# Kernel optimization log

Hardware: AMD Instinct MI355X
Metric: run time of the kernel (lower is better)

Reference implementation:

```python
import jax, jax.numpy as jnp
import numpy as np
import math

CN = [64, 128, 256, 512]
KV = 960  # sum(CN)
B, H, W = 8, 64, 64
HW = H * W
EPS_IN = 1e-5   # InstanceNorm2d eps
EPS_NORM = 1e-12  # F.normalize eps


def _conv(x, w, groups, pad):
    # x: NCHW, w: OIHW (I = C_in/groups)
    return jax.lax.conv_general_dilated(
        x, w, window_strides=(1, 1), padding=pad,
        feature_group_count=groups,
        dimension_numbers=('NCHW', 'OIHW', 'NCHW'))


def _l2norm(x):
    n = jnp.sqrt(jnp.sum(x * x, axis=-1, keepdims=True))
    return x / jnp.maximum(n, EPS_NORM)


def _inorm(a):
    # InstanceNorm2d(affine=False): normalize over last two dims per (b, head)
    mu = jnp.mean(a, axis=(-2, -1), keepdims=True)
    var = jnp.mean((a - mu) ** 2, axis=(-2, -1), keepdims=True)
    return (a - mu) * jax.lax.rsqrt(var + EPS_IN)


def setup_inputs() -> dict:
    key = jax.random.key(0)
    ks = iter(jax.random.split(key, 32))
    d = {}
    d['emb1'] = jax.random.normal(next(ks), (B, CN[0], H, W), jnp.float32)
    d['emb2'] = jax.random.normal(next(ks), (B, CN[1], H, W), jnp.float32)
    d['emb3'] = jax.random.normal(next(ks), (B, CN[2], H, W), jnp.float32)
    d['emb4'] = jax.random.normal(next(ks), (B, CN[3], H, W), jnp.float32)
    d['emb_all'] = jax.random.normal(next(ks), (B, KV, H, W), jnp.float32)
    s = 0.05
    for i, c in enumerate(CN, 1):
        d[f'wm{i}'] = jax.random.normal(next(ks), (c, c, 1, 1), jnp.float32) * s
        d[f'wq{i}'] = jax.random.normal(next(ks), (c, 2, 3, 3), jnp.float32) * s  # groups=c//2
        d[f'wp{i}'] = jax.random.normal(next(ks), (c, c, 1, 1), jnp.float32) * s
    d['wmk'] = jax.random.normal(next(ks), (KV, KV, 1, 1), jnp.float32) * s
    d['wmv'] = jax.random.normal(next(ks), (KV, KV, 1, 1), jnp.float32) * s
    d['wk'] = jax.random.normal(next(ks), (KV, 1, 3, 3), jnp.float32) * s  # depthwise
    d['wv'] = jax.random.normal(next(ks), (KV, 1, 3, 3), jnp.float32) * s
    return d


def reference(emb1, emb2, emb3, emb4, emb_all,
              wm1, wq1, wp1, wm2, wq2, wp2, wm3, wq3, wp3, wm4, wq4, wp4,
              wmk, wmv, wk, wv):
    b, _, h, w = emb1.shape
    scale = 1.0 / math.sqrt(KV)

    def make_q(emb, wm, wq, c):
        q = _conv(_conv(emb, wm, 1, 'VALID'), wq, c // 2, 'SAME')
        q = q.reshape(b, 1, c, h * w)  # head=1
        return _l2norm(q)

    k = _conv(_conv(emb_all, wmk, 1, 'VALID'), wk, KV, 'SAME').reshape(b, 1, KV, h * w)
    v = _conv(_conv(emb_all, wmv, 1, 'VALID'), wv, KV, 'SAME').reshape(b, 1, KV, h * w)
    k = _l2norm(k)

    outs = []
    for emb, wm, wq, wp, c in ((emb1, wm1, wq1, wp1, CN[0]),
                               (emb2, wm2, wq2, wp2, CN[1]),
                               (emb3, wm3, wq3, wp3, CN[2]),
                               (emb4, wm4, wq4, wp4, CN[3])):
        q = make_q(emb, wm, wq, c)                         # b 1 c hw
        attn = jnp.einsum('bhcn,bhdn->bhcd', q, k) * scale  # b 1 c KV
        probs = jax.nn.softmax(_inorm(attn), axis=-1)
        out = jnp.einsum('bhcd,bhdn->bhcn', probs, v)       # b 1 c hw
        out = out.mean(axis=1).reshape(b, c, h, w)          # head mean (head=1)
        outs.append(_conv(out, wp, 1, 'VALID'))
    return tuple(outs)
```

## Files before the change

### kernel.cpp

```cpp
#include <hip/hip_runtime.h>
#include <hip/hip_bf16.h>
#include <math.h>

typedef long long i64;
typedef __hip_bfloat16 bf16;

#define HW 4096
#define KVC 960
#define BATCH 8

using bf8 = __attribute__((ext_vector_type(8))) short;
using f32x4 = __attribute__((ext_vector_type(4))) float;

__device__ __forceinline__ float bf2f(unsigned short u) {
    union { unsigned int i; float f; } c; c.i = ((unsigned int)u) << 16; return c.f;
}
__device__ __forceinline__ float tof(bf16 v) { return __bfloat162float(v); }
__device__ __forceinline__ unsigned short f2bs(float f) {
    bf16 h = __float2bfloat16(f); return *reinterpret_cast<unsigned short*>(&h);
}
__device__ __forceinline__ unsigned short tobs(float f) { return f2bs(f); }
__device__ __forceinline__ unsigned short tobs(bf16 v) { return *reinterpret_cast<unsigned short*>(&v); }
__device__ __forceinline__ void store1(float* p, float v) { *p = v; }
__device__ __forceinline__ void store1(bf16* p, float v) { *p = __float2bfloat16(v); }

__device__ __forceinline__ void gl_lds16(const void* g, void* l) {
    __builtin_amdgcn_global_load_lds(
        (const __attribute__((address_space(1))) void*)g,
        (__attribute__((address_space(3))) void*)l,
        16, 0, 0);
}

template<typename TC>
__global__ __launch_bounds__(256)
void gemm_bt(const bf16* __restrict__ A, int lda, i64 aBatch,
             const bf16* __restrict__ B, int ldb, i64 bBatch,
             TC* __restrict__ C, int ldc, i64 cBatch,
             int M, int N, int K, float alpha)
{
    __shared__ __align__(16) short As[128 * 32];
    __shared__ __align__(16) short Bs[128 * 32];

    const int bz = blockIdx.z;
    const int m0 = blockIdx.y * 128;
    const int n0 = blockIdx.x * 128;
    const int tid  = threadIdx.x;
    const int lane = tid & 63;
    const int wave = tid >> 6;
    const int wm = (wave & 1) * 64;
    const int wn = (wave >> 1) * 64;
    const int quad = lane >> 4;
    const int l16  = lane & 15;

    const bf16* Ab = A + (i64)bz * aBatch;
    const bf16* Bb = B + (i64)bz * bBatch;

    const int srow = lane >> 2;
    const int scol = (lane & 3) * 8;

    int ar0 = m0 + wave * 16 + srow;       if (ar0 >= M) ar0 = M - 1;
    int ar1 = m0 + 64 + wave * 16 + srow;  if (ar1 >= M) ar1 = M - 1;
    int br0 = n0 + wave * 16 + srow;       if (br0 >= N) br0 = N - 1;
    int br1 = n0 + 64 + wave * 16 + srow;  if (br1 >= N) br1 = N - 1;
    const bf16* pa0 = Ab + (i64)ar0 * lda + scol;
    const bf16* pa1 = Ab + (i64)ar1 * lda + scol;
    const bf16* pb0 = Bb + (i64)br0 * ldb + scol;
    const bf16* pb1 = Bb + (i64)br1 * ldb + scol;

    short* la0 = As + wave * 512;
    short* la1 = As + 2048 + wave * 512;
    short* lb0 = Bs + wave * 512;
    short* lb1 = Bs + 2048 + wave * 512;

    f32x4 acc[4][4] = {};

    for (int k0 = 0; k0 < K; k0 += 32) {
        gl_lds16(pa0 + k0, la0);
        gl_lds16(pa1 + k0, la1);
        gl_lds16(pb0 + k0, lb0);
        gl_lds16(pb1 + k0, lb1);
        __syncthreads();

        bf8 af[4], bfr[4];
        #pragma unroll
        for (int mt = 0; mt < 4; ++mt)
            af[mt] = *(const bf8*)(As + (wm + mt * 16 + l16) * 32 + quad * 8);
        #pragma unroll
        for (int nt = 0; nt < 4; ++nt)
            bfr[nt] = *(const bf8*)(Bs + (wn + nt * 16 + l16) * 32 + quad * 8);
        #pragma unroll
        for (int mt = 0; mt < 4; ++mt)
            #pragma unroll
            for (int nt = 0; nt < 4; ++nt)
                acc[mt][nt] = __builtin_amdgcn_mfma_f32_16x16x32_bf16(
                    af[mt], bfr[nt], acc[mt][nt], 0, 0, 0);
        __syncthreads();
    }

    const i64 cb = (i64)bz * cBatch;
    #pragma unroll
    for (int mt = 0; mt < 4; ++mt) {
        #pragma unroll
        for (int r = 0; r < 4; ++r) {
            const int row = m0 + wm + mt * 16 + quad * 4 + r;
            if (row >= M) continue;
            const i64 rb = cb + (i64)row * ldc;
            #pragma unroll
            for (int nt = 0; nt < 4; ++nt) {
                const int col = n0 + wn + nt * 16 + l16;
                if (col < N) store1(C + rb + col, alpha * acc[mt][nt][r]);
            }
        }
    }
}

template<typename T>
__global__ __launch_bounds__(256)
void transpose_to_bt(const T* __restrict__ in, bf16* __restrict__ outT, int C)
{
    __shared__ unsigned short t[64][66];
    const int b  = blockIdx.z;
    const int n0 = blockIdx.x * 64;
    const int c0 = blockIdx.y * 64;
    const int tx = threadIdx.x & 63, ty = threadIdx.x >> 6;
    const T* ip = in + ((i64)b * C + c0) * (i64)HW + n0;
    #pragma unroll
    for (int i = 0; i < 16; ++i) {
        const int r = ty + i * 4;
        t[r][tx] = tobs(ip[(i64)r * HW + tx]);
    }
    __syncthreads();
    bf16* op = outT + ((i64)b * HW + n0) * (i64)C + c0;
    #pragma unroll
    for (int i = 0; i < 16; ++i) {
        const int r = ty + i * 4;
        *(unsigned short*)(op + (i64)r * C + tx) = t[tx][r];
    }
}

__global__ __launch_bounds__(256)
void cvt_weights(const float* __restrict__ s0, const float* __restrict__ s1,
                 const float* __restrict__ s2, const float* __restrict__ s3,
                 const float* __restrict__ s4, const float* __restrict__ s5,
                 const float* __restrict__ s6, const float* __restrict__ s7,
                 const float* __restrict__ s8, const float* __restrict__ s9,
                 bf16* __restrict__ wb)
{
    const int i = (blockIdx.x * 256 + threadIdx.x) * 4;
    if (i >= 2539520) return;
    const float* src; int off;
    if      (i <  921600) { src = s0; off = 0;       }
    else if (i < 1843200) { src = s1; off = 921600;  }
    else if (i < 1847296) { src = s2; off = 1843200; }
    else if (i < 1863680) { src = s3; off = 1847296; }
    else if (i < 1929216) { src = s4; off = 1863680; }
    else if (i < 2191360) { src = s5; off = 1929216; }
    else if (i < 2195456) { src = s6; off = 2191360; }
    else if (i < 2211840) { src = s7; off = 2195456; }
    else if (i < 2277376) { src = s8; off = 2211840; }
    else                  { src = s9; off = 2277376; }
    const float4 v = *(const float4*)(src + (i - off));
    ushort4 o;
    o.x = f2bs(v.x); o.y = f2bs(v.y); o.z = f2bs(v.z); o.w = f2bs(v.w);
    *(ushort4*)((unsigned short*)wb + i) = o;
}

template<bool NORM>
__global__ __launch_bounds__(256)
void dw3x3_fused(const bf16* __restrict__ in, const float* __restrict__ w,
                 bf16* __restrict__ out, int C)
{
    __shared__ __align__(16) unsigned short img[4096];
    __shared__ float red[4];
    __shared__ float sinv;
    const int bc = blockIdx.x;
    const int c = bc % C;
    const int tid = threadIdx.x;
    const int lane = tid & 63, wave = tid >> 6;
    const bf16* ip = in + (i64)bc * HW;
    gl_lds16(ip + wave * 512 + lane * 8, img + wave * 512);
    gl_lds16(ip + (4 + wave) * 512 + lane * 8, img + (4 + wave) * 512);

    const float* wp9 = w + c * 9;
    float wr[9];
    #pragma unroll
    for (int i = 0; i < 9; ++i) wr[i] = wp9[i];
    __syncthreads();

    const int x0 = (tid & 15) * 4, y0 = (tid >> 4) * 4;
    float fin[6][6];
    #pragma unroll
    for (int r = 0; r < 6; ++r) {
        const int yy = y0 - 1 + r;
        const int yc = (yy < 0) ? 0 : (yy > 63 ? 63 : yy);
        const bool yok = (yy >= 0) && (yy <= 63);
        #pragma unroll
        for (int cc = 0; cc < 6; ++cc) {
            const int xx = x0 - 1 + cc;
            const int xc = (xx < 0) ? 0 : (xx > 63 ? 63 : xx);
            const float v = bf2f(img[yc * 64 + xc]);
            fin[r][cc] = (yok && xx >= 0 && xx <= 63) ? v : 0.f;
        }
    }

    float o[4][4];
    float ss = 0.f;
    #pragma unroll
    for (int r = 0; r < 4; ++r) {
        #pragma unroll
        for (int cc = 0; cc < 4; ++cc) {
            float s = 0.f;
            #pragma unroll
            for (int dy = 0; dy < 3; ++dy)
                #pragma unroll
                for (int dx = 0; dx < 3; ++dx)
                    s = fmaf(wr[dy * 3 + dx], fin[r + dy][cc + dx], s);
            o[r][cc] = s;
            ss = fmaf(s, s, ss);
        }
    }

    float inv = 1.f;
    if (NORM) {
        #pragma unroll
        for (int off = 32; off > 0; off >>= 1) ss += __shfl_down(ss, off);
        const int wid = tid >> 6;
        if (lane == 0) red[wid] = ss;
        __syncthreads();
        if (tid == 0) {
            const float t = red[0] + red[1] + red[2] + red[3];
            sinv = 1.0f / fmaxf(sqrtf(t), 1e-12f);
        }
        __syncthreads();
        inv = sinv;
    }

    bf16* op = out + (i64)bc * HW;
    #pragma unroll
    for (int r = 0; r < 4; ++r) {
        ushort4 pk;
        pk.x = f2bs(o[r][0] * inv);
        pk.y = f2bs(o[r][1] * inv);
        pk.z = f2bs(o[r][2] * inv);
        pk.w = f2bs(o[r][3] * inv);
        *(ushort4*)(op + (y0 + r) * 64 + x0) = pk;
    }
}

__global__ __launch_bounds__(256)
void gconv3x3_fused(const bf16* __restrict__ in, const float* __restrict__ w,
                    bf16* __restrict__ outAll, int C, int cstart)
{
    __shared__ __align__(16) unsigned short img[8192];
    __shared__ float red[2][4];
    __shared__ float sinv[2];
    const int nb = C >> 1;
    const int b = blockIdx.x / nb;
    const int g = blockIdx.x % nb;
    const int tid = threadIdx.x, lane = tid & 63, wave = tid >> 6;
    const bf16* ip = in + ((i64)b * C + 2 * g) * HW;
    #pragma unroll
    for (int it = 0; it < 4; ++it)
        gl_lds16(ip + (it * 4 + wave) * 512 + lane * 8, img + (it * 4 + wave) * 512);

    const float* wp = w + g * 36;
    float wr[36];
    #pragma unroll
    for (int i = 0; i < 36; ++i) wr[i] = wp[i];
    __syncthreads();

    const int x0 = (tid & 15) * 4, y0 = (tid >> 4) * 4;
    float fin[2][6][6];
    #pragma unroll
    for (int ic = 0; ic < 2; ++ic) {
        #pragma unroll
        for (int r = 0; r < 6; ++r) {
            const int yy = y0 - 1 + r;
            const int yc = (yy < 0) ? 0 : (yy > 63 ? 63 : yy);
            const bool yok = (yy >= 0) && (yy <= 63);
            #pragma unroll
            for (int cc = 0; cc < 6; ++cc) {
                const int xx = x0 - 1 + cc;
                const int xc = (xx < 0) ? 0 : (xx > 63 ? 63 : xx);
                const float v = bf2f(img[ic * 4096 + yc * 64 + xc]);
                fin[ic][r][cc] = (yok && xx >= 0 && xx <= 63) ? v : 0.f;
            }
        }
    }

    float o[2][4][4];
    float ss0 = 0.f, ss1 = 0.f;
    #pragma unroll
    for (int oc = 0; oc < 2; ++oc) {
        #pragma unroll
        for (int r = 0; r < 4; ++r) {
            #pragma unroll
            for (int cc = 0; cc < 4; ++cc) {
                float s = 0.f;
                #pragma unroll
                for (int ic = 0; ic < 2; ++ic)
                    #pragma unroll
                    for (int dy = 0; dy < 3; ++dy)
                        #pragma unroll
                        for (int dx = 0; dx < 3; ++dx)
                            s = fmaf(wr[oc * 18 + ic * 9 + dy * 3 + dx],
                                     fin[ic][r + dy][cc + dx], s);
                o[oc][r][cc] = s;
                if (oc == 0) ss0 = fmaf(s, s, ss0); else ss1 = fmaf(s, s, ss1);
            }
        }
    }

    #pragma unroll
    for (int off = 32; off > 0; off >>= 1) {
        ss0 += __shfl_down(ss0, off);
        ss1 += __shfl_down(ss1, off);
    }
    const int wid = tid >> 6;
    if (lane == 0) { red[0][wid] = ss0; red[1][wid] = ss1; }
    __syncthreads();
    if (tid == 0) {
        const float t0 = red[0][0] + red[0][1] + red[0][2] + red[0][3];
        const float t1 = red[1][0] + red[1][1] + red[1][2] + red[1][3];
        sinv[0] = 1.0f / fmaxf(sqrtf(t0), 1e-12f);
        sinv[1] = 1.0f / fmaxf(sqrtf(t1), 1e-12f);
    }
    __syncthreads();

    #pragma unroll
    for (int oc = 0; oc < 2; ++oc) {
        const float inv = sinv[oc];
        bf16* op = outAll + ((i64)b * KVC + cstart + 2 * g + oc) * HW;
        #pragma unroll
        for (int r = 0; r < 4; ++r) {
            ushort4 pk;
            pk.x = f2bs(o[oc][r][0] * inv);
            pk.y = f2bs(o[oc][r][1] * inv);
            pk.z = f2bs(o[oc][r][2] * inv);
            pk.w = f2bs(o[oc][r][3] * inv);
            *(ushort4*)(op + (y0 + r) * 64 + x0) = pk;
        }
    }
}

__global__ __launch_bounds__(256)
void inorm_partial(const float* __restrict__ a, float* __restrict__ part)
{
    const int b = blockIdx.x, ch = blockIdx.y, br = blockIdx.z;
    const int CC[4] = {64, 128, 256, 512};
    const int CS[4] = {0, 64, 192, 448};
    const int c = CC[br], cs = CS[br];
    const int csh = 31 - __clz(c);
    const int cmask = c - 1;
    const float* p = a + (i64)b * (KVC * KVC) + (i64)(ch * 30) * KVC + cs;
    const int tot = 30 * c;
    float s = 0.f, s2 = 0.f;
    for (int i = threadIdx.x; i < tot; i += 256) {
        const float v = p[(i64)(i >> csh) * KVC + (i & cmask)];
        s += v;
        s2 = fmaf(v, v, s2);
    }
    #pragma unroll
    for (int o = 32; o > 0; o >>= 1) { s += __shfl_down(s, o); s2 += __shfl_down(s2, o); }
    __shared__ float r1[4], r2[4];
    const int lane = threadIdx.x & 63, wid = threadIdx.x >> 6;
    if (lane == 0) { r1[wid] = s; r2[wid] = s2; }
    __syncthreads();
    if (threadIdx.x == 0) {
        part[((br * 8 + b) * 32 + ch) * 2 + 0] = r1[0] + r1[1] + r1[2] + r1[3];
        part[((br * 8 + b) * 32 + ch) * 2 + 1] = r2[0] + r2[1] + r2[2] + r2[3];
    }
}

__global__ __launch_bounds__(64)
void inorm_finish(const float* __restrict__ part, float* __restrict__ stats)
{
    const int b = blockIdx.x, br = blockIdx.y;
    const int i = threadIdx.x;
    float s = 0.f, s2 = 0.f;
    if (i < 32) {
        s  = part[((br * 8 + b) * 32 + i) * 2 + 0];
        s2 = part[((br * 8 + b) * 32 + i) * 2 + 1];
    }
    #pragma unroll
    for (int o = 16; o > 0; o >>= 1) { s += __shfl_down(s, o); s2 += __shfl_down(s2, o); }
    if (i == 0) {
        const int CC[4] = {64, 128, 256, 512};
        const float n = (float)(CC[br] * KVC);
        const float mu = s / n;
        const float var = s2 / n - mu * mu;
        stats[(br * 8 + b) * 2 + 0] = mu;
        stats[(br * 8 + b) * 2 + 1] = rsqrtf(var + 1e-5f);
    }
}

__global__ __launch_bounds__(256)
void softmax_cols(const float* __restrict__ a, bf16* __restrict__ p,
                  const float* __restrict__ stats)
{
    const int b  = blockIdx.y;
    const int cb = blockIdx.x * 64;
    const int br = (cb >= 448) ? 3 : (cb >= 192) ? 2 : (cb >= 64) ? 1 : 0;
    const int tx = threadIdx.x & 63, ty = threadIdx.x >> 6;
    const float mu = stats[(br * 8 + b) * 2 + 0];
    const float rs = stats[(br * 8 + b) * 2 + 1];
    const i64 base = (i64)b * (KVC * KVC) + cb + tx;

    float mx = -1e30f;
    for (int r = ty; r < KVC; r += 4)
        mx = fmaxf(mx, a[base + (i64)r * KVC]);
    __shared__ float red[4][64];
    red[ty][tx] = mx;
    __syncthreads();
    mx = fmaxf(fmaxf(red[0][tx], red[1][tx]), fmaxf(red[2][tx], red[3][tx]));
    const float M = (mx - mu) * rs;

    float se = 0.f;
    for (int r = ty; r < KVC; r += 4)
        se += __expf((a[base + (i64)r * KVC] - mu) * rs - M);
    __syncthreads();
    red[ty][tx] = se;
    __syncthreads();
    const float S = red[0][tx] + red[1][tx] + red[2][tx] + red[3][tx];
    const float inv = 1.0f / S;

    for (int r = ty; r < KVC; r += 4) {
        const float e = __expf((a[base + (i64)r * KVC] - mu) * rs - M);
        p[base + (i64)r * KVC] = __float2bfloat16(e * inv);
    }
}

extern "C" void kernel_launch(void* const* d_in, const int* in_sizes, int n_in,
                              void* d_out, int out_size, void* d_ws, size_t ws_size,
                              hipStream_t stream)
{
    (void)in_sizes; (void)n_in; (void)out_size; (void)ws_size;

    const float* emb[4]  = {(const float*)d_in[0], (const float*)d_in[1],
                            (const float*)d_in[2], (const float*)d_in[3]};
    const float* emb_all = (const float*)d_in[4];
    const float* wq[4]   = {(const float*)d_in[6], (const float*)d_in[9],
                            (const float*)d_in[12], (const float*)d_in[15]};
    const float* wmk = (const float*)d_in[17];
    const float* wmv = (const float*)d_in[18];
    const float* wk  = (const float*)d_in[19];
    const float* wv  = (const float*)d_in[20];
    float* out = (float*)d_out;

    char* ws = (char*)d_ws;
    bf16*  kb     = (bf16*)ws;
    bf16*  vT     = (bf16*)(ws + 62914560LL);
    bf16*  Q      = (bf16*)(ws + 125829120LL);
    char*  Sr     = ws + 188743680LL;
    bf16*  sb     = (bf16*)Sr;
    bf16*  embT   = (bf16*)(Sr + 33554432LL);
    float* attnT  = (float*)Sr;
    bf16*  probsT = (bf16*)(Sr + 29491200LL);
    bf16*  probsP = (bf16*)(Sr + 44236800LL);
    bf16*  wb     = (bf16*)(ws + 255852544LL);
    float* part   = (float*)(ws + 260931584LL);
    float* stats  = (float*)(ws + 260939776LL);

    const dim3 blk(256);
    const float scale = (float)(1.0 / sqrt((double)KVC));
    const int CNl[4] = {64, 128, 256, 512};
    const int CSl[4] = {0, 64, 192, 448};
    const i64 wmOff[4] = {1843200, 1847296, 1863680, 1929216};
    const i64 wpOff[4] = {2191360, 2195456, 2211840, 2277376};

    cvt_weights<<<2480, blk, 0, stream>>>(wmk, wmv,
        (const float*)d_in[5], (const float*)d_in[8],
        (const float*)d_in[11], (const float*)d_in[14],
        (const float*)d_in[7], (const float*)d_in[10],
        (const float*)d_in[13], (const float*)d_in[16], wb);

    transpose_to_bt<float><<<dim3(64, 15, BATCH), blk, 0, stream>>>(emb_all, Q, KVC);

    gemm_bt<bf16><<<dim3(32, 8, BATCH), blk, 0, stream>>>(
        wb, KVC, 0, Q, KVC, (i64)HW * KVC, sb, HW, (i64)KVC * HW,
        KVC, HW, KVC, 1.0f);
    dw3x3_fused<true><<<BATCH * KVC, blk, 0, stream>>>(sb, wk, kb, KVC);

    gemm_bt<bf16><<<dim3(32, 8, BATCH), blk, 0, stream>>>(
        wb + 921600, KVC, 0, Q, KVC, (i64)HW * KVC, sb, HW, (i64)KVC * HW,
        KVC, HW, KVC, 1.0f);
    dw3x3_fused<false><<<BATCH * KVC, blk, 0, stream>>>(sb, wv, Q, KVC);
    transpose_to_bt<bf16><<<dim3(64, 15, BATCH), blk, 0, stream>>>(Q, vT, KVC);

    for (int i = 0; i < 4; ++i) {
        const int c = CNl[i], cs = CSl[i];
        transpose_to_bt<float><<<dim3(64, c / 64, BATCH), blk, 0, stream>>>(
            emb[i], embT, c);
        gemm_bt<bf16><<<dim3(32, (c + 127) / 128, BATCH), blk, 0, stream>>>(
            wb + wmOff[i], c, 0, embT, c, (i64)HW * c, sb, HW, (i64)c * HW,
            c, HW, c, 1.0f);
        gconv3x3_fused<<<BATCH * (c / 2), blk, 0, stream>>>(sb, wq[i], Q, c, cs);
    }

    gemm_bt<float><<<dim3(8, 8, BATCH), blk, 0, stream>>>(
        kb, HW, (i64)KVC * HW, Q, HW, (i64)KVC * HW, attnT, KVC, (i64)KVC * KVC,
        KVC, KVC, HW, scale);

    inorm_partial<<<dim3(BATCH, 32, 4), blk, 0, stream>>>(attnT, part);
    inorm_finish<<<dim3(BATCH, 4), 64, 0, stream>>>(part, stats);
    softmax_cols<<<dim3(15, BATCH), blk, 0, stream>>>(attnT, probsT, stats);

    i64 ooff = 0;
    for (int i = 0; i < 4; ++i) {
        const int c = CNl[i], cs = CSl[i];
        gemm_bt<bf16><<<dim3(8, (c + 127) / 128, BATCH), blk, 0, stream>>>(
            wb + wpOff[i], c, 0, probsT + cs, KVC, (i64)KVC * KVC,
            probsP, KVC, (i64)c * KVC, c, KVC, c, 1.0f);
        gemm_bt<float><<<dim3(32, (c + 127) / 128, BATCH), blk, 0, stream>>>(
            probsP, KVC, (i64)c * KVC, vT, KVC, (i64)HW * KVC,
            out + ooff, HW, (i64)c * HW, c, HW, KVC, 1.0f);
        ooff += (i64)BATCH * c * HW;
    }
}
```

Before: 1.205 ms.

## Compute attention scores row-major, softmax per row, then transpose probabilities

The Q·K GEMM now writes attention with query channels as rows instead of transposed, so instance-norm statistics and softmax read contiguous float4 rows rather than strided columns. The softmax is restructured to one block per row with wave-shuffle reductions, so each element is loaded once. A new bf16 square-transpose kernel rebuilds the transposed probability layout the downstream GEMMs expect. This adds one extra launch and one extra pass over the probability matrix in exchange for coalesced access and far more parallel blocks in the softmax stage.

After: 1.042 ms. 1.16x faster.

```diff
diff --git a/kernel.cpp b/kernel.cpp
--- a/kernel.cpp
+++ b/kernel.cpp
@@ -135,6 +135,29 @@
     for (int i = 0; i < 16; ++i) {
         const int r = ty + i * 4;
         *(unsigned short*)(op + (i64)r * C + tx) = t[tx][r];
+    }
+}
+
+__global__ __launch_bounds__(256)
+void transpose_sq(const bf16* __restrict__ in, bf16* __restrict__ out)
+{
+    __shared__ unsigned short t[64][66];
+    const int b  = blockIdx.z;
+    const int r0 = blockIdx.y * 64;
+    const int c0 = blockIdx.x * 64;
+    const int tx = threadIdx.x & 63, ty = threadIdx.x >> 6;
+    const bf16* ip = in + ((i64)b * KVC + r0) * KVC + c0;
+    #pragma unroll
+    for (int i = 0; i < 16; ++i) {
+        const int r = ty + i * 4;
+        t[r][tx] = tobs(ip[(i64)r * KVC + tx]);
+    }
+    __syncthreads();
+    bf16* op = out + ((i64)b * KVC + c0) * KVC + r0;
+    #pragma unroll
+    for (int i = 0; i < 16; ++i) {
+        const int r = ty + i * 4;
+        *(unsigned short*)(op + (i64)r * KVC + tx) = t[tx][r];
     }
 }
 
@@ -349,16 +372,15 @@
     const int b = blockIdx.x, ch = blockIdx.y, br = blockIdx.z;
     const int CC[4] = {64, 128, 256, 512};
     const int CS[4] = {0, 64, 192, 448};
-    const int c = CC[br], cs = CS[br];
-    const int csh = 31 - __clz(c);
-    const int cmask = c - 1;
-    const float* p = a + (i64)b * (KVC * KVC) + (i64)(ch * 30) * KVC + cs;
-    const int tot = 30 * c;
+    const int c = CC[br];
+    const int n4 = c * 30 / 4;
+    const float4* p = (const float4*)(a + (i64)b * (KVC * KVC)
+                                        + (i64)CS[br] * KVC) + (i64)ch * n4;
     float s = 0.f, s2 = 0.f;
-    for (int i = threadIdx.x; i < tot; i += 256) {
-        const float v = p[(i64)(i >> csh) * KVC + (i & cmask)];
-        s += v;
-        s2 = fmaf(v, v, s2);
+    for (int i = threadIdx.x; i < n4; i += 256) {
+        const float4 v = p[i];
+        s += v.x + v.y + v.z + v.w;
+        s2 += v.x * v.x + v.y * v.y + v.z * v.z + v.w * v.w;
     }
     #pragma unroll
     for (int o = 32; o > 0; o >>= 1) { s += __shfl_down(s, o); s2 += __shfl_down(s2, o); }
@@ -395,38 +417,55 @@
 }
 
 __global__ __launch_bounds__(256)
-void softmax_cols(const float* __restrict__ a, bf16* __restrict__ p,
+void softmax_rows(const float* __restrict__ a, bf16* __restrict__ p,
                   const float* __restrict__ stats)
 {
-    const int b  = blockIdx.y;
-    const int cb = blockIdx.x * 64;
-    const int br = (cb >= 448) ? 3 : (cb >= 192) ? 2 : (cb >= 64) ? 1 : 0;
-    const int tx = threadIdx.x & 63, ty = threadIdx.x >> 6;
+    const int q = blockIdx.x, b = blockIdx.y;
+    const int br = (q >= 448) ? 3 : (q >= 192) ? 2 : (q >= 64) ? 1 : 0;
     const float mu = stats[(br * 8 + b) * 2 + 0];
     const float rs = stats[(br * 8 + b) * 2 + 1];
-    const i64 base = (i64)b * (KVC * KVC) + cb + tx;
-
+    const i64 base = ((i64)b * KVC + q) * KVC;
+    const int t = threadIdx.x;
+    const bool act = t < 240;
+
+    float x[4];
     float mx = -1e30f;
-    for (int r = ty; r < KVC; r += 4)
-        mx = fmaxf(mx, a[base + (i64)r * KVC]);
-    __shared__ float red[4][64];
-    red[ty][tx] = mx;
-    __syncthreads();
-    mx = fmaxf(fmaxf(red[0][tx], red[1][tx]), fmaxf(red[2][tx], red[3][tx]));
-    const float M = (mx - mu) * rs;
-
+    if (act) {
+        const float4 v = ((const float4*)(a + base))[t];
+        x[0] = (v.x - mu) * rs; x[1] = (v.y - mu) * rs;
+        x[2] = (v.z - mu) * rs; x[3] = (v.w - mu) * rs;
+        mx = fmaxf(fmaxf(x[0], x[1]), fmaxf(x[2], x[3]));
+    }
+    __shared__ float red[4];
+    __shared__ float bM, bS;
+    const int lane = t & 63, wid = t >> 6;
+    #pragma unroll
+    for (int o = 32; o > 0; o >>= 1) mx = fmaxf(mx, __shfl_down(mx, o));
+    if (lane == 0) red[wid] = mx;
+    __syncthreads();
+    if (t == 0) bM = fmaxf(fmaxf(red[0], red[1]), fmaxf(red[2], red[3]));
+    __syncthreads();
+    const float M = bM;
+
+    float e[4];
     float se = 0.f;
-    for (int r = ty; r < KVC; r += 4)
-        se += __expf((a[base + (i64)r * KVC] - mu) * rs - M);
-    __syncthreads();
-    red[ty][tx] = se;
-    __syncthreads();
-    const float S = red[0][tx] + red[1][tx] + red[2][tx] + red[3][tx];
-    const float inv = 1.0f / S;
-
-    for (int r = ty; r < KVC; r += 4) {
-        const float e = __expf((a[base + (i64)r * KVC] - mu) * rs - M);
-        p[base + (i64)r * KVC] = __float2bfloat16(e * inv);
+    if (act) {
+        #pragma unroll
+        for (int j = 0; j < 4; ++j) { e[j] = __expf(x[j] - M); se += e[j]; }
+    }
+    #pragma unroll
+    for (int o = 32; o > 0; o >>= 1) se += __shfl_down(se, o);
+    if (lane == 0) red[wid] = se;
+    __syncthreads();
+    if (t == 0) bS = red[0] + red[1] + red[2] + red[3];
+    __syncthreads();
+    const float inv = 1.0f / bS;
+
+    if (act) {
+        ushort4 o4;
+        o4.x = f2bs(e[0] * inv); o4.y = f2bs(e[1] * inv);
+        o4.z = f2bs(e[2] * inv); o4.w = f2bs(e[3] * inv);
+        ((ushort4*)((unsigned short*)p + base))[t] = o4;
     }
 }
 
@@ -454,9 +493,10 @@
     char*  Sr     = ws + 188743680LL;
     bf16*  sb     = (bf16*)Sr;
     bf16*  embT   = (bf16*)(Sr + 33554432LL);
-    float* attnT  = (float*)Sr;
+    float* attn   = (float*)Sr;
     bf16*  probsT = (bf16*)(Sr + 29491200LL);
     bf16*  probsP = (bf16*)(Sr + 44236800LL);
+    bf16*  pbuf   = (bf16*)(Sr + 52101120LL);
     bf16*  wb     = (bf16*)(ws + 255852544LL);
     float* part   = (float*)(ws + 260931584LL);
     float* stats  = (float*)(ws + 260939776LL);
@@ -498,12 +538,13 @@
     }
 
     gemm_bt<float><<<dim3(8, 8, BATCH), blk, 0, stream>>>(
-        kb, HW, (i64)KVC * HW, Q, HW, (i64)KVC * HW, attnT, KVC, (i64)KVC * KVC,
+        Q, HW, (i64)KVC * HW, kb, HW, (i64)KVC * HW, attn, KVC, (i64)KVC * KVC,
         KVC, KVC, HW, scale);
 
-    inorm_partial<<<dim3(BATCH, 32, 4), blk, 0, stream>>>(attnT, part);
+    inorm_partial<<<dim3(BATCH, 32, 4), blk, 0, stream>>>(attn, part);
     inorm_finish<<<dim3(BATCH, 4), 64, 0, stream>>>(part, stats);
-    softmax_cols<<<dim3(15, BATCH), blk, 0, stream>>>(attnT, probsT, stats);
+    softmax_rows<<<dim3(KVC, BATCH), blk, 0, stream>>>(attn, pbuf, stats);
+    transpose_sq<<<dim3(15, 15, BATCH), blk, 0, stream>>>(pbuf, probsT);
 
     i64 ooff = 0;
     for (int i = 0; i < 4; ++i) {
```
